# Optimization experiments

Measured on AMD Instinct MI355X. Metric: run time of the kernel, lower is better.

## Reference

```python
import jax, jax.numpy as jnp
import numpy as np

K = 15  # kNN neighbors, matches init kwarg


def _knn_edges(x, k):
    # brute-force kNN, flow='target_to_source': row = center node, col = neighbor
    sq = jnp.sum(x * x, axis=-1)
    d2 = sq[:, None] - 2.0 * (x @ x.T) + sq[None, :]          # [N,N]
    n = x.shape[0]
    d2 = jnp.where(jnp.eye(n, dtype=bool), jnp.inf, d2)        # exclude self-loops
    _, idx = jax.lax.top_k(-d2, k)                             # [N,k] nearest
    row = jnp.repeat(jnp.arange(n), k)
    col = idx.reshape(-1)
    return jnp.stack([row, col])                               # [2, N*k]


def _scatter_softmax(a, seg, n):
    m = jax.ops.segment_max(a, seg, num_segments=n)
    m = jnp.where(jnp.isfinite(m), m, 0.0)
    e = jnp.exp(a - m[seg])
    s = jax.ops.segment_sum(e, seg, num_segments=n)
    return e / s[seg]


def _devconv(x, edges, W_theta, b_theta, W_phi, b_phi):
    # DevConv (neural mesh simplification): W_phi . max_{j in N(i)} W_theta(x_i - x_j)
    row, col = edges[0], edges[1]
    h = (x[row] - x[col]) @ W_theta.T + b_theta                # [E, H]
    agg = jax.ops.segment_max(h, row, num_segments=x.shape[0])  # [N, H]
    agg = jnp.where(jnp.isfinite(agg), agg, 0.0)               # guard empty rows
    return agg @ W_phi.T + b_phi


def setup_inputs() -> dict:
    key = jax.random.key(0)
    ks = jax.random.split(key, 8)
    N, E, H, C = 4096, 65536, 64, 3
    x = jax.random.normal(ks[0], (N, C), dtype=jnp.float32)
    edge_index = jax.random.randint(ks[1], (2, E), 0, N, dtype=jnp.int64)
    s_in, s_h = 1.0 / np.sqrt(C), 1.0 / np.sqrt(H)
    return {
        "x": x,
        "edge_index": edge_index,
        "W_theta": jax.random.normal(ks[2], (H, C), dtype=jnp.float32) * s_in,
        "b_theta": jnp.zeros((H,), dtype=jnp.float32),
        "W_phi": jax.random.normal(ks[3], (H, H), dtype=jnp.float32) * s_h,
        "b_phi": jnp.zeros((H,), dtype=jnp.float32),
        "W_q": jax.random.normal(ks[4], (H, H), dtype=jnp.float32) * s_h,
        "W_k": jax.random.normal(ks[5], (H, H), dtype=jnp.float32) * s_h,
    }


def reference(x, edge_index, W_theta, b_theta, W_phi, b_phi, W_q, W_k):
    n = x.shape[0]
    knn = _knn_edges(x, K)
    extended = jnp.concatenate([edge_index, knn], axis=1)
    feats = _devconv(x, extended, W_theta, b_theta, W_phi, b_phi)  # [N, H]
    row, col = edge_index[0], edge_index[1]
    q = feats @ W_q.T
    kf = feats @ W_k.T
    attn = jnp.sum(q[row] * kf[col], axis=-1)                  # [E]
    scores = _scatter_softmax(attn, row, n)                     # [E]
    # S, A as dense NxN (duplicates summed, matching sparse coalescing)
    S = jnp.zeros((n, n), dtype=x.dtype).at[row, col].add(scores)
    A = jnp.zeros((n, n), dtype=x.dtype).at[row, col].add(1.0)
    A_s = S @ A @ S.T                                           # simplified adjacency
    return A_s
```

## Files before the change

kernel.cpp:

```cpp
#include <hip/hip_runtime.h>
#include <math.h>

#define HN 64
#define KNN 15

__device__ __forceinline__ unsigned fenc(float f){
  unsigned u = __float_as_uint(f);
  return (u & 0x80000000u) ? ~u : (u | 0x80000000u);
}

__device__ __forceinline__ unsigned long long u64min(unsigned long long a, unsigned long long b){
  return a < b ? a : b;
}
__device__ __forceinline__ unsigned long long shfl_xor_u64(unsigned long long v, int mask){
  unsigned lo = (unsigned)v, hi = (unsigned)(v >> 32);
  lo = __shfl_xor((int)lo, mask, 64);
  hi = __shfl_xor((int)hi, mask, 64);
  return ((unsigned long long)hi << 32) | lo;
}

__device__ __forceinline__ void edge_load(const void* ei, int E, int n, int e, int& r, int& c){
  const long long* L = (const long long*)ei;
  long long vr = L[e];
  bool ok = (vr >= 0 && vr < (long long)n);
  unsigned long long bal = __ballot(ok);
  unsigned long long act = __ballot(true);
  if (bal == act){
    r = (int)vr;
    c = (int)L[E + e];
  } else {
    const int* I = (const int*)ei;
    r = I[e];
    c = I[E + e];
  }
}

__global__ void __launch_bounds__(256) k_mega(
    const float* __restrict__ x, const float* __restrict__ Wt, const void* ei,
    float* __restrict__ y, int* __restrict__ knn_cols,
    int* __restrict__ cnt, int* __restrict__ ccnt,
    int N, int E, int nbY, int nbC){
  __shared__ unsigned denc[4096];
  __shared__ unsigned long long mk[256];
  int b = blockIdx.x, t = threadIdx.x;
  if (b < nbY){
    int gid = b * 256 + t;
    if (gid < N * HN){
      int nn = gid >> 6, h = gid & 63;
      y[gid] = x[nn*3] * Wt[h*3] + x[nn*3+1] * Wt[h*3+1] + x[nn*3+2] * Wt[h*3+2];
    }
    return;
  }
  if (b < nbY + nbC){
    int e = (b - nbY) * 256 + t;
    if (e < E){
      int r, c;
      edge_load(ei, E, N, e, r, c);
      atomicAdd(&cnt[r], 1);
      atomicAdd(&ccnt[c], 1);
    }
    return;
  }
  int i = b - nbY - nbC;
  float xi0 = x[i*3], xi1 = x[i*3+1], xi2 = x[i*3+2];
  float sqi = xi0*xi0 + xi1*xi1 + xi2*xi2;
  unsigned long long best = ~0ULL;
  #pragma unroll
  for (int m = 0; m < 16; ++m){
    int j = t + 256*m;
    float a = x[j*3], bb = x[j*3+1], c = x[j*3+2];
    float sqj = a*a + bb*bb + c*c;
    float dot = xi0*a + xi1*bb + xi2*c;
    float d2 = (sqi - 2.0f*dot) + sqj;
    unsigned e = (j == i) ? 0xFFFFFFFFu : fenc(d2);
    denc[j] = e;
    best = u64min(best, ((unsigned long long)e << 32) | (unsigned)j);
  }
  mk[t] = best;
  __syncthreads();
  if (t >= 64) return;
  unsigned long long k0 = mk[t], k1 = mk[t+64], k2 = mk[t+128], k3 = mk[t+192];
  for (int m = 0; m < KNN; ++m){
    unsigned long long mm = u64min(u64min(k0, k1), u64min(k2, k3));
    #pragma unroll
    for (int off = 1; off < 64; off <<= 1)
      mm = u64min(mm, shfl_xor_u64(mm, off));
    int j = (int)(mm & 0xFFFFFFFFu);
    if (t == 0) knn_cols[i*KNN + m] = j;
    if ((j & 63) == t){
      int slot = j & 255;
      denc[j] = 0xFFFFFFFFu;
      unsigned long long nb = ~0ULL;
      #pragma unroll
      for (int m2 = 0; m2 < 16; ++m2){
        int jj = slot + 256*m2;
        nb = u64min(nb, ((unsigned long long)denc[jj] << 32) | (unsigned)jj);
      }
      int kreg = (j >> 6) & 3;
      if (kreg == 0) k0 = nb; else if (kreg == 1) k1 = nb;
      else if (kreg == 2) k2 = nb; else k3 = nb;
    }
  }
}

__global__ void k_scan2(const int* __restrict__ cnt, int* __restrict__ ptr,
                        const int* __restrict__ ccnt, int* __restrict__ cptr,
                        int2* __restrict__ rinfo, int2* __restrict__ cinfo, int n){
  __shared__ int part[1024];
  const int* src = (blockIdx.x == 0) ? cnt : ccnt;
  int* dst = (blockIdx.x == 0) ? ptr : cptr;
  int t = threadIdx.x;
  int base = t * 4;
  int a0 = src[base], a1 = src[base+1], a2 = src[base+2], a3 = src[base+3];
  int s = a0 + a1 + a2 + a3;
  part[t] = s;
  __syncthreads();
  for (int off = 1; off < 1024; off <<= 1){
    int v = (t >= off) ? part[t - off] : 0;
    __syncthreads();
    part[t] += v;
    __syncthreads();
  }
  int excl = part[t] - s;
  int v0 = excl, v1 = excl + a0, v2 = excl + a0 + a1, v3 = excl + a0 + a1 + a2;
  dst[base]   = v0;
  dst[base+1] = v1;
  dst[base+2] = v2;
  dst[base+3] = v3;
  if (t == 1023) dst[n] = part[1023];
  if (blockIdx.x == 0){
    rinfo[base]   = make_int2(v0 + KNN*base,     a0);
    rinfo[base+1] = make_int2(v1 + KNN*(base+1), a1);
    rinfo[base+2] = make_int2(v2 + KNN*(base+2), a2);
    rinfo[base+3] = make_int2(v3 + KNN*(base+3), a3);
  } else {
    cinfo[base]   = make_int2(v0, a0);
    cinfo[base+1] = make_int2(v1, a1);
    cinfo[base+2] = make_int2(v2, a2);
    cinfo[base+3] = make_int2(v3, a3);
  }
}

__global__ void k_fill(const void* ei, const int* __restrict__ ptr,
                       int* __restrict__ fillo, const int* __restrict__ cnt,
                       const int* __restrict__ knncols, int* __restrict__ ecol,
                       int N, int E, int nbE){
  int b = blockIdx.x, t = threadIdx.x;
  if (b < nbE){
    int e = b * 256 + t;
    if (e < E){
      int r, c;
      edge_load(ei, E, N, e, r, c);
      int pos = ptr[r] + KNN*r + atomicAdd(&fillo[r], 1);
      ecol[pos] = c;
    }
  } else {
    int gid = (b - nbE) * 256 + t;
    if (gid < N * KNN){
      int i = gid / KNN, m = gid - i * KNN;
      ecol[ptr[i] + KNN*i + cnt[i] + m] = knncols[gid];
    }
  }
}

__global__ void k_dev(const int* __restrict__ ptr, const int* __restrict__ ecol,
                      const float* __restrict__ y, const float* __restrict__ bt,
                      const float* __restrict__ Wp, const float* __restrict__ bp,
                      const float* __restrict__ Wq, const float* __restrict__ Wk,
                      float* __restrict__ q, float* __restrict__ kf, int n){
  __shared__ float sag[256];
  __shared__ float sft[256];
  int t = threadIdx.x;
  int i = blockIdx.x * 4 + (t >> 6);
  int h = t & 63;
  int beg = ptr[i] + KNN*i;
  int end = ptr[i+1] + KNN*(i+1);
  float m = INFINITY;
  for (int idx = beg; idx < end; ++idx)
    m = fminf(m, y[ecol[idx]*HN + h]);
  sag[t] = y[i*HN + h] + bt[h] - m;
  __syncthreads();
  int nn = t >> 6;
  float acc = bp[h];
  #pragma unroll 8
  for (int c = 0; c < HN; ++c) acc += sag[nn*HN + c] * Wp[h*HN + c];
  sft[t] = acc;
  __syncthreads();
  float aq = 0.f, ak = 0.f;
  #pragma unroll 8
  for (int c = 0; c < HN; ++c){
    float f = sft[nn*HN + c];
    aq += f * Wq[h*HN + c];
    ak += f * Wk[h*HN + c];
  }
  size_t o = (size_t)blockIdx.x * 256 + t;
  q[o] = aq;
  kf[o] = ak;
}

__global__ void __launch_bounds__(256) k_rowattn(
    const int* __restrict__ ptr, const int2* __restrict__ cinfo,
    const int* __restrict__ ecol, const float* __restrict__ q,
    const float* __restrict__ kf, float* __restrict__ sval,
    int2* __restrict__ scp, int2* __restrict__ csp,
    int* __restrict__ cfill, int n){
  int t = threadIdx.x;
  int lane = t & 63;
  int r = blockIdx.x * 4 + (t >> 6);
  if (r >= n) return;
  int base = ptr[r];
  int deg = ptr[r+1] - base;
  if (deg == 0) return;
  int ebase = base + KNN*r;
  float4 qv[16];
  const float4* qr = (const float4*)(q + (size_t)r*HN);
  #pragma unroll
  for (int m = 0; m < 16; ++m) qv[m] = qr[m];
  float mx = -INFINITY;
  for (int s = lane; s < deg; s += 64){
    int c = ecol[ebase + s];
    const float4* kc = (const float4*)(kf + (size_t)c*HN);
    float acc = 0.f;
    #pragma unroll
    for (int m = 0; m < 16; ++m){
      float4 b = kc[m];
      acc += qv[m].x*b.x + qv[m].y*b.y + qv[m].z*b.z + qv[m].w*b.w;
    }
    sval[base + s] = acc;
    mx = fmaxf(mx, acc);
  }
  #pragma unroll
  for (int off = 1; off < 64; off <<= 1) mx = fmaxf(mx, __shfl_xor(mx, off, 64));
  float lsum = 0.f;
  for (int s = lane; s < deg; s += 64){
    float e = expf(sval[base + s] - mx);
    sval[base + s] = e;
    lsum += e;
  }
  #pragma unroll
  for (int off = 1; off < 64; off <<= 1) lsum += __shfl_xor(lsum, off, 64);
  for (int s = lane; s < deg; s += 64){
    float v = sval[base + s] / lsum;
    int c = ecol[ebase + s];
    scp[base + s] = make_int2(c, __float_as_int(v));
    int pos = cinfo[c].x + atomicAdd(&cfill[c], 1);
    csp[pos] = make_int2(r, __float_as_int(v));
  }
}

__global__ void __launch_bounds__(512) k_prod(
    const int* __restrict__ ptr, const int2* __restrict__ scp,
    const int2* __restrict__ rinfo, const int* __restrict__ ecol,
    const int2* __restrict__ cinfo, const int2* __restrict__ csp,
    float* __restrict__ out, int n){
  __shared__ float orow[2][4096];
  int t = threadIdx.x;
  int half = t >> 8;
  int tt = t & 255;
  int lane = t & 63;
  int w = (t >> 6) & 3;
  int i = blockIdx.x * 2 + half;
  float4 z = {0.f, 0.f, 0.f, 0.f};
  float4* o4 = (float4*)orow[half];
  #pragma unroll
  for (int ch = 0; ch < 4; ++ch) o4[ch*256 + tt] = z;
  __syncthreads();
  int base = ptr[i];
  int len = ptr[i+1] - base;
  int qs = lane >> 2, rq = lane & 3;
  float* my = orow[half];
  for (int p = w; p < len; p += 4){
    int2 kv = scp[base + p];
    float v = __int_as_float(kv.y);
    int2 ri = rinfo[kv.x];
    for (int qq = qs; qq < ri.y; qq += 16){
      int l = ecol[ri.x + qq];
      int2 ci = cinfo[l];
      for (int rr = rq; rr < ci.y; rr += 4){
        int2 e2 = csp[ci.x + rr];
        atomicAdd(&my[e2.x], v * __int_as_float(e2.y));
      }
    }
  }
  __syncthreads();
  float4* dst = (float4*)(out + (size_t)i * n);
  #pragma unroll
  for (int ch = 0; ch < 4; ++ch) dst[ch*256 + tt] = o4[ch*256 + tt];
}

extern "C" void kernel_launch(void* const* d_in, const int* in_sizes, int n_in,
                              void* d_out, int out_size, void* d_ws, size_t ws_size,
                              hipStream_t stream) {
  const float* x   = (const float*)d_in[0];
  const void*  ei  = d_in[1];
  const float* Wt  = (const float*)d_in[2];
  const float* bt  = (const float*)d_in[3];
  const float* Wp  = (const float*)d_in[4];
  const float* bp  = (const float*)d_in[5];
  const float* Wq  = (const float*)d_in[6];
  const float* Wk  = (const float*)d_in[7];
  float* out = (float*)d_out;

  const int N = in_sizes[0] / 3;
  const int E = in_sizes[1] / 2;

  char* p = (char*)d_ws;
  auto alloc = [&](size_t bytes) -> void* {
    void* r = (void*)p;
    p += (bytes + 255) & ~(size_t)255;
    return r;
  };
  int*      ctr     = (int*)  alloc((size_t)4*N*4);
  int*      cnt     = ctr;
  int*      ccnt    = ctr + N;
  int*      cfill   = ctr + 2*N;
  int*      fillo   = ctr + 3*N;

  float*    y       = (float*)alloc((size_t)N*HN*4);
  float*    q       = (float*)alloc((size_t)N*HN*4);
  float*    kf      = (float*)alloc((size_t)N*HN*4);
  int*      ptrb    = (int*)  alloc((size_t)(N+1)*4);
  int*      cptrb   = (int*)  alloc((size_t)(N+1)*4);
  int2*     rinfo   = (int2*) alloc((size_t)N*8);
  int2*     cinfo   = (int2*) alloc((size_t)N*8);
  int*      ecol    = (int*)  alloc((size_t)(E + N*KNN)*4);
  float*    sval    = (float*)alloc((size_t)E*4);
  int2*     scp     = (int2*) alloc((size_t)E*8);
  int2*     csp     = (int2*) alloc((size_t)E*8);
  int*      knncols = (int*)  alloc((size_t)N*KNN*4);

  hipMemsetAsync(ctr, 0, (size_t)4*N*4, stream);

  int nbY = (N*HN + 255)/256;
  int nbC = (E + 255)/256;
  int nbK = (N*KNN + 255)/256;

  k_mega<<<nbY + nbC + N, 256, 0, stream>>>(x, Wt, ei, y, knncols, cnt, ccnt,
                                            N, E, nbY, nbC);
  k_scan2<<<2, 1024, 0, stream>>>(cnt, ptrb, ccnt, cptrb, rinfo, cinfo, N);
  k_fill<<<nbC + nbK, 256, 0, stream>>>(ei, ptrb, fillo, cnt, knncols, ecol,
                                        N, E, nbC);
  k_dev<<<N/4, 256, 0, stream>>>(ptrb, ecol, y, bt, Wp, bp, Wq, Wk, q, kf, N);
  k_rowattn<<<N/4, 256, 0, stream>>>(ptrb, cinfo, ecol, q, kf, sval, scp, csp,
                                     cfill, N);
  k_prod<<<N/2, 512, 0, stream>>>(ptrb, scp, rinfo, ecol, cinfo, csp, out, N);
}
```

Measured before the change: 291.3 us.

## Precompute flattened A·S^T lists per column node before sparse triple product

Replaces the nested triple-loop product kernel with a three-stage pipeline. The first stage counts the total A·S^T contributions per node, the second does an exclusive scan of those counts, and the third materializes each node's (col, weight) list into a flat buffer. The apply kernel then walks one contiguous list per S entry with all 256 threads, avoiding the irregular nested loops and load imbalance of the old kernel. This costs two extra launches, a large temporary buffer (fixed 4M entries, which could overflow on other inputs), and extra global traffic to write and reread the lists.

After: 305.8 us. +5.0%, slower.

```diff
diff --git a/kernel.cpp b/kernel.cpp
--- a/kernel.cpp
+++ b/kernel.cpp
@@ -203,7 +203,7 @@
     const int* __restrict__ ecol, const float* __restrict__ q,
     const float* __restrict__ kf, float* __restrict__ sval,
     int2* __restrict__ scp, int2* __restrict__ csp,
-    int* __restrict__ cfill, int n){
+    int* __restrict__ cfill, int* __restrict__ tlen, int n){
   int t = threadIdx.x;
   int lane = t & 63;
   int r = blockIdx.x * 4 + (t >> 6);
@@ -239,53 +239,121 @@
   }
   #pragma unroll
   for (int off = 1; off < 64; off <<= 1) lsum += __shfl_xor(lsum, off, 64);
+  int tsum = 0;
   for (int s = lane; s < deg; s += 64){
     float v = sval[base + s] / lsum;
     int c = ecol[ebase + s];
     scp[base + s] = make_int2(c, __float_as_int(v));
-    int pos = cinfo[c].x + atomicAdd(&cfill[c], 1);
+    int2 ci = cinfo[c];
+    int pos = ci.x + atomicAdd(&cfill[c], 1);
     csp[pos] = make_int2(r, __float_as_int(v));
-  }
-}
-
-__global__ void __launch_bounds__(512) k_prod(
-    const int* __restrict__ ptr, const int2* __restrict__ scp,
+    tsum += ci.y;
+  }
+  #pragma unroll
+  for (int off = 1; off < 64; off <<= 1) tsum += __shfl_xor(tsum, off, 64);
+  if (lane == 0) tlen[r] = tsum;
+}
+
+__global__ void k_scant(const int* __restrict__ tlen, int2* __restrict__ tinfo, int n){
+  __shared__ int part[1024];
+  int t = threadIdx.x;
+  int base = t * 4;
+  int a0 = tlen[base], a1 = tlen[base+1], a2 = tlen[base+2], a3 = tlen[base+3];
+  int s = a0 + a1 + a2 + a3;
+  part[t] = s;
+  __syncthreads();
+  for (int off = 1; off < 1024; off <<= 1){
+    int v = (t >= off) ? part[t - off] : 0;
+    __syncthreads();
+    part[t] += v;
+    __syncthreads();
+  }
+  int excl = part[t] - s;
+  tinfo[base]   = make_int2(excl, a0);
+  tinfo[base+1] = make_int2(excl + a0, a1);
+  tinfo[base+2] = make_int2(excl + a0 + a1, a2);
+  tinfo[base+3] = make_int2(excl + a0 + a1 + a2, a3);
+}
+
+__global__ void __launch_bounds__(256) k_tbuild(
     const int2* __restrict__ rinfo, const int* __restrict__ ecol,
     const int2* __restrict__ cinfo, const int2* __restrict__ csp,
+    const int2* __restrict__ tinfo, int2* __restrict__ tlist, int n){
+  __shared__ int pre[65];
+  __shared__ int csrc[64];
+  int k = blockIdx.x, t = threadIdx.x, lane = t & 63;
+  int2 ri = rinfo[k];
+  int running = tinfo[k].x;
+  for (int l0 = 0; l0 < ri.y; l0 += 64){
+    int chunk = min(64, ri.y - l0);
+    __syncthreads();
+    if (t < 64){
+      int v = 0, src = 0;
+      if (lane < chunk){
+        int c = ecol[ri.x + l0 + lane];
+        int2 ci = cinfo[c];
+        v = ci.y; src = ci.x;
+      }
+      csrc[lane] = src;
+      int ps = v;
+      #pragma unroll
+      for (int off = 1; off < 64; off <<= 1){
+        int o = __shfl_up(ps, off, 64);
+        if (lane >= off) ps += o;
+      }
+      pre[lane + 1] = ps;
+      if (lane == 0) pre[0] = 0;
+    }
+    __syncthreads();
+    int total = pre[chunk];
+    for (int d = t; d < total; d += 256){
+      int lo = 0, hi = chunk - 1;
+      while (lo < hi){
+        int mid = (lo + hi + 1) >> 1;
+        if (pre[mid] <= d) lo = mid; else hi = mid - 1;
+      }
+      tlist[running + d] = csp[csrc[lo] + (d - pre[lo])];
+    }
+    running += total;
+  }
+}
+
+__global__ void __launch_bounds__(256) k_papply(
+    const int* __restrict__ ptr, const int2* __restrict__ scp,
+    const int2* __restrict__ tinfo, const int2* __restrict__ tlist,
     float* __restrict__ out, int n){
-  __shared__ float orow[2][4096];
-  int t = threadIdx.x;
-  int half = t >> 8;
-  int tt = t & 255;
-  int lane = t & 63;
-  int w = (t >> 6) & 3;
-  int i = blockIdx.x * 2 + half;
+  __shared__ float orow[4096];
+  __shared__ float svv[64];
+  __shared__ int2  sti[64];
+  int i = blockIdx.x, t = threadIdx.x;
   float4 z = {0.f, 0.f, 0.f, 0.f};
-  float4* o4 = (float4*)orow[half];
-  #pragma unroll
-  for (int ch = 0; ch < 4; ++ch) o4[ch*256 + tt] = z;
-  __syncthreads();
+  float4* o4 = (float4*)orow;
+  #pragma unroll
+  for (int ch = 0; ch < 4; ++ch) o4[ch*256 + t] = z;
   int base = ptr[i];
   int len = ptr[i+1] - base;
-  int qs = lane >> 2, rq = lane & 3;
-  float* my = orow[half];
-  for (int p = w; p < len; p += 4){
-    int2 kv = scp[base + p];
-    float v = __int_as_float(kv.y);
-    int2 ri = rinfo[kv.x];
-    for (int qq = qs; qq < ri.y; qq += 16){
-      int l = ecol[ri.x + qq];
-      int2 ci = cinfo[l];
-      for (int rr = rq; rr < ci.y; rr += 4){
-        int2 e2 = csp[ci.x + rr];
-        atomicAdd(&my[e2.x], v * __int_as_float(e2.y));
+  for (int p0 = 0; p0 < len; p0 += 64){
+    int chunk = min(64, len - p0);
+    __syncthreads();
+    if (t < chunk){
+      int2 kv = scp[base + p0 + t];
+      svv[t] = __int_as_float(kv.y);
+      sti[t] = tinfo[kv.x];
+    }
+    __syncthreads();
+    for (int p = 0; p < chunk; ++p){
+      float v = svv[p];
+      int2 ti = sti[p];
+      for (int d = t; d < ti.y; d += 256){
+        int2 e = tlist[ti.x + d];
+        atomicAdd(&orow[e.x], v * __int_as_float(e.y));
       }
     }
   }
   __syncthreads();
   float4* dst = (float4*)(out + (size_t)i * n);
   #pragma unroll
-  for (int ch = 0; ch < 4; ++ch) dst[ch*256 + tt] = o4[ch*256 + tt];
+  for (int ch = 0; ch < 4; ++ch) dst[ch*256 + t] = o4[ch*256 + t];
 }
 
 extern "C" void kernel_launch(void* const* d_in, const int* in_sizes, int n_in,
@@ -310,11 +378,12 @@
     p += (bytes + 255) & ~(size_t)255;
     return r;
   };
-  int*      ctr     = (int*)  alloc((size_t)4*N*4);
+  int*      ctr     = (int*)  alloc((size_t)5*N*4);
   int*      cnt     = ctr;
   int*      ccnt    = ctr + N;
   int*      cfill   = ctr + 2*N;
   int*      fillo   = ctr + 3*N;
+  int*      tlen    = ctr + 4*N;
 
   float*    y       = (float*)alloc((size_t)N*HN*4);
   float*    q       = (float*)alloc((size_t)N*HN*4);
@@ -323,13 +392,15 @@
   int*      cptrb   = (int*)  alloc((size_t)(N+1)*4);
   int2*     rinfo   = (int2*) alloc((size_t)N*8);
   int2*     cinfo   = (int2*) alloc((size_t)N*8);
+  int2*     tinfo   = (int2*) alloc((size_t)N*8);
   int*      ecol    = (int*)  alloc((size_t)(E + N*KNN)*4);
   float*    sval    = (float*)alloc((size_t)E*4);
   int2*     scp     = (int2*) alloc((size_t)E*8);
   int2*     csp     = (int2*) alloc((size_t)E*8);
   int*      knncols = (int*)  alloc((size_t)N*KNN*4);
-
-  hipMemsetAsync(ctr, 0, (size_t)4*N*4, stream);
+  int2*     tlist   = (int2*) alloc((size_t)4*1024*1024*8);
+
+  hipMemsetAsync(ctr, 0, (size_t)5*N*4, stream);
 
   int nbY = (N*HN + 255)/256;
   int nbC = (E + 255)/256;
@@ -342,6 +413,8 @@
                                         N, E, nbC);
   k_dev<<<N/4, 256, 0, stream>>>(ptrb, ecol, y, bt, Wp, bp, Wq, Wk, q, kf, N);
   k_rowattn<<<N/4, 256, 0, stream>>>(ptrb, cinfo, ecol, q, kf, sval, scp, csp,
-                                     cfill, N);
-  k_prod<<<N/2, 512, 0, stream>>>(ptrb, scp, rinfo, ecol, cinfo, csp, out, N);
-}
+                                     cfill, tlen, N);
+  k_scant<<<1, 1024, 0, stream>>>(tlen, tinfo, N);
+  k_tbuild<<<N, 256, 0, stream>>>(rinfo, ecol, cinfo, csp, tinfo, tlist, N);
+  k_papply<<<N, 256, 0, stream>>>(ptrb, scp, tinfo, tlist, out, N);
+}
```

## Precompute sparse A·S^T rows then apply S via compacted lists

Applied to the files above, without the earlier changes.

Splits the triple product S·A·S^T into two stages. The first builds a compacted sparse row T = A·S^T per node, capped at MAXT entries, and merges duplicates through shared-memory tag-based conflict rounds. The second accumulates S·T per output row without atomics. This removes the nested three-level traversal with shared atomics in the old product kernel. In exchange it adds a large workspace, an extra launch, and silently truncates rows with more than 768 entries, which could be wrong for denser inputs.

After: 311.9 us. +7.1%, slower.

```diff
diff --git a/kernel.cpp b/kernel.cpp
--- a/kernel.cpp
+++ b/kernel.cpp
@@ -3,6 +3,7 @@
 
 #define HN 64
 #define KNN 15
+#define MAXT 768
 
 __device__ __forceinline__ unsigned fenc(float f){
   unsigned u = __float_as_uint(f);
@@ -243,49 +244,126 @@
     float v = sval[base + s] / lsum;
     int c = ecol[ebase + s];
     scp[base + s] = make_int2(c, __float_as_int(v));
-    int pos = cinfo[c].x + atomicAdd(&cfill[c], 1);
+    int2 ci = cinfo[c];
+    int pos = ci.x + atomicAdd(&cfill[c], 1);
     csp[pos] = make_int2(r, __float_as_int(v));
   }
 }
 
-__global__ void __launch_bounds__(512) k_prod(
-    const int* __restrict__ ptr, const int2* __restrict__ scp,
+__global__ void __launch_bounds__(256) k_tbuild(
     const int2* __restrict__ rinfo, const int* __restrict__ ecol,
     const int2* __restrict__ cinfo, const int2* __restrict__ csp,
+    int2* __restrict__ tlist, int* __restrict__ tcnt, int n){
+  __shared__ float Drow[4096];
+  __shared__ int   tag[4096];
+  __shared__ int   pre[65];
+  __shared__ int   csrc[64];
+  __shared__ int   wsum[4];
+  int k = blockIdx.x, t = threadIdx.x, lane = t & 63, wid = t >> 6;
+  float4* D4 = (float4*)Drow;
+  float4 fz = {0.f, 0.f, 0.f, 0.f};
+  #pragma unroll
+  for (int j = 0; j < 4; ++j) D4[j*256 + t] = fz;
+  int2 ri = rinfo[k];
+  int nseg = min(ri.y, 64);
+  if (t < 64){
+    int v = 0, src = 0;
+    if (lane < nseg){
+      int c = ecol[ri.x + lane];
+      int2 ci = cinfo[c];
+      v = ci.y; src = ci.x;
+    }
+    csrc[lane] = src;
+    int ps = v;
+    #pragma unroll
+    for (int off = 1; off < 64; off <<= 1){
+      int o = __shfl_up(ps, off, 64);
+      if (lane >= off) ps += o;
+    }
+    pre[lane + 1] = ps;
+    if (lane == 0) pre[0] = 0;
+  }
+  __syncthreads();
+  int total = min(pre[nseg], MAXT);
+  int er[3]; float ev[3]; bool edone[3];
+  #pragma unroll
+  for (int j = 0; j < 3; ++j){
+    int d = t + 256*j;
+    edone[j] = true;
+    er[j] = 0; ev[j] = 0.f;
+    if (d < total){
+      int lo = 0, hi = nseg - 1;
+      while (lo < hi){
+        int mid = (lo + hi + 1) >> 1;
+        if (pre[mid] <= d) lo = mid; else hi = mid - 1;
+      }
+      int2 e = csp[csrc[lo] + (d - pre[lo])];
+      er[j] = e.x; ev[j] = __int_as_float(e.y); edone[j] = false;
+    }
+  }
+  int wr[3]; int wn = 0;
+  int round = 0;
+  while (true){
+    #pragma unroll
+    for (int j = 0; j < 3; ++j) if (!edone[j]) tag[er[j]] = t + 256*j;
+    __syncthreads();
+    bool any = false;
+    #pragma unroll
+    for (int j = 0; j < 3; ++j) if (!edone[j]){
+      if (tag[er[j]] == t + 256*j){
+        Drow[er[j]] += ev[j];
+        edone[j] = true;
+        if (round == 0) wr[wn++] = er[j];
+      } else any = true;
+    }
+    ++round;
+    if (__syncthreads_count(any ? 1 : 0) == 0) break;
+    if (round >= MAXT) break;
+  }
+  int v = wn;
+  #pragma unroll
+  for (int off = 1; off < 64; off <<= 1){
+    int o = __shfl_up(v, off, 64);
+    if (lane >= off) v += o;
+  }
+  if (lane == 63) wsum[wid] = v;
+  __syncthreads();
+  int base0 = 0;
+  #pragma unroll
+  for (int w = 0; w < 4; ++w) if (w < wid) base0 += wsum[w];
+  int excl = base0 + v - wn;
+  int2* trow = tlist + (size_t)k * MAXT;
+  #pragma unroll
+  for (int j = 0; j < 3; ++j) if (j < wn)
+    trow[excl + j] = make_int2(wr[j], __float_as_int(Drow[wr[j]]));
+  if (t == 0) tcnt[k] = wsum[0] + wsum[1] + wsum[2] + wsum[3];
+}
+
+__global__ void __launch_bounds__(64) k_papply(
+    const int* __restrict__ ptr, const int2* __restrict__ scp,
+    const int2* __restrict__ tlist, const int* __restrict__ tcnt,
     float* __restrict__ out, int n){
-  __shared__ float orow[2][4096];
-  int t = threadIdx.x;
-  int half = t >> 8;
-  int tt = t & 255;
-  int lane = t & 63;
-  int w = (t >> 6) & 3;
-  int i = blockIdx.x * 2 + half;
+  __shared__ float orow[4096];
+  int i = blockIdx.x, t = threadIdx.x;
+  float4* o4 = (float4*)orow;
   float4 z = {0.f, 0.f, 0.f, 0.f};
-  float4* o4 = (float4*)orow[half];
-  #pragma unroll
-  for (int ch = 0; ch < 4; ++ch) o4[ch*256 + tt] = z;
-  __syncthreads();
-  int base = ptr[i];
-  int len = ptr[i+1] - base;
-  int qs = lane >> 2, rq = lane & 3;
-  float* my = orow[half];
-  for (int p = w; p < len; p += 4){
+  #pragma unroll
+  for (int j = 0; j < 16; ++j) o4[j*64 + t] = z;
+  int base = ptr[i], len = ptr[i+1] - base;
+  for (int p = 0; p < len; ++p){
     int2 kv = scp[base + p];
+    int k = kv.x;
     float v = __int_as_float(kv.y);
-    int2 ri = rinfo[kv.x];
-    for (int qq = qs; qq < ri.y; qq += 16){
-      int l = ecol[ri.x + qq];
-      int2 ci = cinfo[l];
-      for (int rr = rq; rr < ci.y; rr += 4){
-        int2 e2 = csp[ci.x + rr];
-        atomicAdd(&my[e2.x], v * __int_as_float(e2.y));
-      }
-    }
-  }
-  __syncthreads();
+    int tc = tcnt[k];
+    const int2* trow = tlist + (size_t)k * MAXT;
+    for (int d = t; d < tc; d += 64){
+      int2 e = trow[d];
+      orow[e.x] += v * __int_as_float(e.y);
+    }
+  }
   float4* dst = (float4*)(out + (size_t)i * n);
   #pragma unroll
-  for (int ch = 0; ch < 4; ++ch) dst[ch*256 + tt] = o4[ch*256 + tt];
+  for (int j = 0; j < 16; ++j) dst[j*64 + t] = o4[j*64 + t];
 }
 
 extern "C" void kernel_launch(void* const* d_in, const int* in_sizes, int n_in,
@@ -328,6 +406,8 @@
   int2*     scp     = (int2*) alloc((size_t)E*8);
   int2*     csp     = (int2*) alloc((size_t)E*8);
   int*      knncols = (int*)  alloc((size_t)N*KNN*4);
+  int*      tcnt    = (int*)  alloc((size_t)N*4);
+  int2*     tlist   = (int2*) alloc((size_t)N*MAXT*8);
 
   hipMemsetAsync(ctr, 0, (size_t)4*N*4, stream);
 
@@ -343,5 +423,6 @@
   k_dev<<<N/4, 256, 0, stream>>>(ptrb, ecol, y, bt, Wp, bp, Wq, Wk, q, kf, N);
   k_rowattn<<<N/4, 256, 0, stream>>>(ptrb, cinfo, ecol, q, kf, sval, scp, csp,
                                      cfill, N);
-  k_prod<<<N/2, 512, 0, stream>>>(ptrb, scp, rinfo, ecol, cinfo, csp, out, N);
-}
+  k_tbuild<<<N, 256, 0, stream>>>(rinfo, ecol, cinfo, csp, tlist, tcnt, N);
+  k_papply<<<N, 64, 0, stream>>>(ptrb, scp, tlist, tcnt, out, N);
+}
```
